# Kernel tuning notes

Measured on AMD Instinct MI355X. Metric: run time of the kernel, lower is better.

## Reference

```python
import jax, jax.numpy as jnp
import numpy as np

IN_DIM, HID, OUT, N_EXTRA, NTASKS, BATCH = 1024, 2048, 10, 3, 10, 4096
LOGSTD_MEAN, LOGSTD_STD = -6.0, 0.1


def setup_inputs() -> dict:
    key = jax.random.key(0)
    ks = jax.random.split(key, 20)
    n = lambda k, s: jax.random.normal(k, s, dtype=jnp.float32)
    return {
        "x": n(ks[0], (BATCH, IN_DIM)),
        # shared layer 0 (in_dim -> hidden)
        "mu_w0": n(ks[1], (HID, IN_DIM)) * (1.0 / np.sqrt(IN_DIM)),
        "ls_w0": LOGSTD_MEAN + LOGSTD_STD * n(ks[2], (HID, IN_DIM)),
        "mu_b0": n(ks[3], (HID,)) * 0.01,
        "ls_b0": LOGSTD_MEAN + LOGSTD_STD * n(ks[4], (HID,)),
        # shared layers 1..3 (hidden -> hidden), stacked
        "mu_w": n(ks[5], (N_EXTRA, HID, HID)) * (1.0 / np.sqrt(HID)),
        "ls_w": LOGSTD_MEAN + LOGSTD_STD * n(ks[6], (N_EXTRA, HID, HID)),
        "mu_b": n(ks[7], (N_EXTRA, HID)) * 0.01,
        "ls_b": LOGSTD_MEAN + LOGSTD_STD * n(ks[8], (N_EXTRA, HID)),
        # per-task heads (hidden -> out), stacked over tasks
        "mu_hw": n(ks[9], (NTASKS, OUT, HID)) * (1.0 / np.sqrt(HID)),
        "ls_hw": LOGSTD_MEAN + LOGSTD_STD * n(ks[10], (NTASKS, OUT, HID)),
        "mu_hb": n(ks[11], (NTASKS, OUT)) * 0.01,
        "ls_hb": LOGSTD_MEAN + LOGSTD_STD * n(ks[12], (NTASKS, OUT)),
        # reparameterization noise (one sample per forward, as in torch module)
        "eps_w0": n(ks[13], (HID, IN_DIM)),
        "eps_b0": n(ks[14], (HID,)),
        "eps_w": n(ks[15], (N_EXTRA, HID, HID)),
        "eps_b": n(ks[16], (N_EXTRA, HID)),
        "eps_hw": n(ks[17], (NTASKS, OUT, HID)),
        "eps_hb": n(ks[18], (NTASKS, OUT)),
        "task": jax.random.randint(ks[19], (BATCH,), 0, NTASKS, dtype=jnp.int64),
    }


def reference(x, mu_w0, ls_w0, mu_b0, ls_b0, mu_w, ls_w, mu_b, ls_b,
              mu_hw, ls_hw, mu_hb, ls_hb,
              eps_w0, eps_b0, eps_w, eps_b, eps_hw, eps_hb, task):
    # BayesianLinear: w = mu + exp(log_sigma) * eps
    w0 = mu_w0 + jnp.exp(ls_w0) * eps_w0          # [HID, IN]
    b0 = mu_b0 + jnp.exp(ls_b0) * eps_b0          # [HID]
    h = jax.nn.relu(x @ w0.T + b0)                # [B, HID]
    for i in range(N_EXTRA):                      # fixed small layer loop
        wi = mu_w[i] + jnp.exp(ls_w[i]) * eps_w[i]
        bi = mu_b[i] + jnp.exp(ls_b[i]) * eps_b[i]
        h = jax.nn.relu(h @ wi.T + bi)
    # multihead: compute every head, zero out non-matching rows (dense masked)
    hw = mu_hw + jnp.exp(ls_hw) * eps_hw          # [T, OUT, HID]
    hb = mu_hb + jnp.exp(ls_hb) * eps_hb          # [T, OUT]
    out_all = jnp.einsum('bh,toh->bto', h, hw) + hb[None]   # [B, T, OUT]
    onehot = (task[:, None] == jnp.arange(NTASKS)[None, :]).astype(h.dtype)
    return jnp.einsum('bto,bt->bo', out_all, onehot)        # [B, OUT]
```

## Files before the change

kernel.cpp:

```cpp
#include <hip/hip_runtime.h>
#include <cstdint>

#define BATCH 4096
#define IN_DIM 1024
#define HID 2048
#define OUT_DIM 10
#define NTASKS 10

typedef __bf16 bf16x8 __attribute__((ext_vector_type(8)));
typedef float f32x4 __attribute__((ext_vector_type(4)));
typedef __attribute__((address_space(3))) uint8_t lds_u8;
typedef const __attribute__((address_space(1))) uint8_t glb_u8;

__device__ __forceinline__ unsigned short f2bf(float f) {
    uint32_t u = __builtin_bit_cast(uint32_t, f);
    u += 0x7fffu + ((u >> 16) & 1u);
    return (unsigned short)(u >> 16);
}

#define C1 1048576u
#define C2 1572864u
#define C3 4718592u
#define C4 4769792u
#define C5 4770304u
#define GLL(src, ldsp) __builtin_amdgcn_global_load_lds((glb_u8*)(src), (lds_u8*)(ldsp), 16, 0, 0)

__global__ __launch_bounds__(256) void bl_stream(
    const float4* __restrict__ x4,
    const float4* __restrict__ m0, const float4* __restrict__ l0, const float4* __restrict__ e0,
    const float4* __restrict__ mw, const float4* __restrict__ lw, const float4* __restrict__ ew,
    const float4* __restrict__ mh, const float4* __restrict__ lh, const float4* __restrict__ eh,
    const float4* __restrict__ mb0, const float4* __restrict__ lb0, const float4* __restrict__ eb0,
    const float4* __restrict__ mb, const float4* __restrict__ lb, const float4* __restrict__ eb,
    const float* __restrict__ mu_hb, const float* __restrict__ ls_hb, const float* __restrict__ eps_hb,
    ushort4* __restrict__ xbf4, ushort4* __restrict__ w0b4, ushort4* __restrict__ wb4,
    float4* __restrict__ hw4, float4* __restrict__ b04, float4* __restrict__ bb4,
    float* __restrict__ hbf)
{
    __shared__ uint8_t sbuf[24576];
    const int tid = threadIdx.x, wv = tid >> 6, ln = tid & 63;

    if (blockIdx.x == 0 && tid < 100)
        hbf[tid] = mu_hb[tid] + __expf(ls_hb[tid]) * eps_hb[tid];

    const int w = blockIdx.x * 4 + wv;
    const int niter = 18 + (w < 832 ? 1 : 0);
    const uint32_t u0 = (uint32_t)(w * 18 + (w < 832 ? w : 832)) * 64u + (uint32_t)ln;
    uint8_t* wl = sbuf + wv * 6144;

    #define SEG_SRC(u, pa, pb, pc)                                               \
        do {                                                                     \
            uint32_t _u = (u);                                                   \
            if (_u < C1)      { pa = x4 + _u; pb = pa; pc = pa; }                \
            else if (_u < C2) { uint32_t v = _u - C1; pa = m0 + v; pb = l0 + v; pc = e0 + v; } \
            else if (_u < C3) { uint32_t v = _u - C2; pa = mw + v; pb = lw + v; pc = ew + v; } \
            else if (_u < C4) { uint32_t v = _u - C3; pa = mh + v; pb = lh + v; pc = eh + v; } \
            else if (_u < C5) { uint32_t v = _u - C4; pa = mb0 + v; pb = lb0 + v; pc = eb0 + v; } \
            else              { uint32_t v = _u - C5; pa = mb + v; pb = lb + v; pc = eb + v; } \
        } while (0)

    {
        const float4 *pa, *pb, *pc;
        SEG_SRC(u0, pa, pb, pc);
        GLL(pa, wl); GLL(pb, wl + 1024); GLL(pc, wl + 2048);
    }

    for (int it = 0; it < niter; ++it) {
        const int cb = it & 1;
        if (it + 1 < niter) {
            const float4 *pa, *pb, *pc;
            SEG_SRC(u0 + (uint32_t)(it + 1) * 64u, pa, pb, pc);
            uint8_t* nb = wl + (cb ^ 1) * 3072;
            GLL(pa, nb); GLL(pb, nb + 1024); GLL(pc, nb + 2048);
            asm volatile("s_waitcnt vmcnt(3)" ::: "memory");
        } else {
            asm volatile("s_waitcnt vmcnt(0)" ::: "memory");
        }
        const uint8_t* rb = wl + cb * 3072;
        const float4 m = *(const float4*)(rb + ln * 16);
        const float4 l = *(const float4*)(rb + 1024 + ln * 16);
        const float4 e = *(const float4*)(rb + 2048 + ln * 16);

        const uint32_t u = u0 + (uint32_t)it * 64u;
        if (u < C1) {
            ushort4 r;
            r.x = f2bf(m.x); r.y = f2bf(m.y); r.z = f2bf(m.z); r.w = f2bf(m.w);
            xbf4[u] = r;
        } else {
            float4 t;
            t.x = m.x + __expf(l.x) * e.x;
            t.y = m.y + __expf(l.y) * e.y;
            t.z = m.z + __expf(l.z) * e.z;
            t.w = m.w + __expf(l.w) * e.w;
            if (u < C3) {
                ushort4 r;
                r.x = f2bf(t.x); r.y = f2bf(t.y); r.z = f2bf(t.z); r.w = f2bf(t.w);
                if (u < C2) w0b4[u - C1] = r; else wb4[u - C2] = r;
            } else {
                if (u < C4) hw4[u - C3] = t;
                else if (u < C5) b04[u - C4] = t;
                else bb4[u - C5] = t;
            }
        }
    }
    #undef SEG_SRC
}

#define BAR()        asm volatile("s_barrier" ::: "memory")
#define WAIT_LGKM0() do { asm volatile("s_waitcnt lgkmcnt(0)" ::: "memory"); __builtin_amdgcn_sched_barrier(0); } while (0)
#define RD_A(m, o)   (*(const bf16x8*)(ldsb + acur + (o) + (m)*2048))
#define RD_B(n, o)   (*(const bf16x8*)(ldsb + bcur + (o) + (n)*2048))
#define MFMA(d, va, vb) d = __builtin_amdgcn_mfma_f32_16x16x32_bf16(va, vb, d, 0, 0, 0)
#define STAGEI(i, kel, sl) \
    __builtin_amdgcn_global_load_lds((glb_u8*)(gsrc[i] + (kel)), \
        (lds_u8*)(ldsb + ldst[i] + (uint32_t)(sl) * smul[i]), 16, 0, 0)

__global__ __launch_bounds__(512, 2) void bl_gemm(
    const unsigned short* __restrict__ A,
    const unsigned short* __restrict__ B,
    const float* __restrict__ bias,
    unsigned short* __restrict__ C,
    int K)
{
    __shared__ unsigned short lds[49152];
    uint8_t* ldsb = (uint8_t*)lds;

    const int tid  = threadIdx.x;
    const int wave = tid >> 6;
    const int lane = tid & 63;
    const int swz = ((blockIdx.x & 7) << 5) | (blockIdx.x >> 3);
    const int bm = swz >> 4;
    const int bn = swz & 15;
    const int wr = wave >> 1;
    const int wc = wave & 1;

    const int lr8 = lane >> 3;
    const int ss  = (lane & 7) ^ lr8;
    const unsigned short* gsrc[6];
    uint32_t ldst[6], smul[6];
    #pragma unroll
    for (int i = 0; i < 6; ++i) {
        const int c = wave * 6 + i;
        if (c < 32) {
            gsrc[i] = A + (size_t)(bm * 256 + c * 8 + lr8) * K + ss * 8;
            ldst[i] = (uint32_t)c * 1024u;
            smul[i] = 32768u;
        } else {
            gsrc[i] = B + (size_t)(bn * 128 + (c - 32) * 8 + lr8) * K + ss * 8;
            ldst[i] = 65536u + (uint32_t)(c - 32) * 1024u;
            smul[i] = 16384u;
        }
    }

    const int rA = wr * 64 + (lane & 15);
    const int rB = wc * 64 + (lane & 15);
    const int ks = lane >> 4;
    const uint32_t aoff0 = (uint32_t)(rA * 128 + ((ks       ^ (rA & 7)) * 16));
    const uint32_t aoff1 = (uint32_t)(rA * 128 + (((4 | ks) ^ (rA & 7)) * 16));
    const uint32_t boff0 = (uint32_t)(rB * 128 + ((ks       ^ (rB & 7)) * 16));
    const uint32_t boff1 = (uint32_t)(rB * 128 + (((4 | ks) ^ (rB & 7)) * 16));

    f32x4 acc[4][4] = {};
    const int NT = K >> 6;

    STAGEI(0, 0, 0); STAGEI(1, 0, 0); STAGEI(2, 0, 0);
    STAGEI(3, 0, 0); STAGEI(4, 0, 0); STAGEI(5, 0, 0);
    __syncthreads();

    for (int t = 0; t < NT; ++t) {
        const int cur = t & 1, nxt = cur ^ 1;
        const uint32_t acur = (uint32_t)cur * 32768u;
        const uint32_t bcur = 65536u + (uint32_t)cur * 16384u;
        const bool pf = (t + 1 < NT);
        const int ktn = (t + 1) << 6;

        bf16x8 a0, a1, a2, a3, b0, b1, b2, b3;

        a0 = RD_A(0, aoff0); a1 = RD_A(1, aoff0);
        b0 = RD_B(0, boff0); b1 = RD_B(1, boff0); b2 = RD_B(2, boff0); b3 = RD_B(3, boff0);
        if (pf) { STAGEI(0, ktn, nxt); STAGEI(1, ktn, nxt); STAGEI(2, ktn, nxt); }
        BAR(); WAIT_LGKM0();
        __builtin_amdgcn_s_setprio(1);
        MFMA(acc[0][0], a0, b0); MFMA(acc[0][1], a0, b1); MFMA(acc[0][2], a0, b2); MFMA(acc[0][3], a0, b3);
        MFMA(acc[1][0], a1, b0); MFMA(acc[1][1], a1, b1); MFMA(acc[1][2], a1, b2); MFMA(acc[1][3], a1, b3);
        __builtin_amdgcn_s_setprio(0);
        BAR();

        a2 = RD_A(2, aoff0); a3 = RD_A(3, aoff0);
        if (pf) { STAGEI(3, ktn, nxt); STAGEI(4, ktn, nxt); STAGEI(5, ktn, nxt); }
        BAR(); WAIT_LGKM0();
        __builtin_amdgcn_s_setprio(1);
        MFMA(acc[2][0], a2, b0); MFMA(acc[2][1], a2, b1); MFMA(acc[2][2], a2, b2); MFMA(acc[2][3], a2, b3);
        MFMA(acc[3][0], a3, b0); MFMA(acc[3][1], a3, b1); MFMA(acc[3][2], a3, b2); MFMA(acc[3][3], a3, b3);
        __builtin_amdgcn_s_setprio(0);
        BAR();

        a0 = RD_A(0, aoff1); a1 = RD_A(1, aoff1);
        b0 = RD_B(0, boff1); b1 = RD_B(1, boff1); b2 = RD_B(2, boff1); b3 = RD_B(3, boff1);
        BAR(); WAIT_LGKM0();
        __builtin_amdgcn_s_setprio(1);
        MFMA(acc[0][0], a0, b0); MFMA(acc[0][1], a0, b1); MFMA(acc[0][2], a0, b2); MFMA(acc[0][3], a0, b3);
        MFMA(acc[1][0], a1, b0); MFMA(acc[1][1], a1, b1); MFMA(acc[1][2], a1, b2); MFMA(acc[1][3], a1, b3);
        __builtin_amdgcn_s_setprio(0);
        BAR();

        a2 = RD_A(2, aoff1); a3 = RD_A(3, aoff1);
        BAR(); WAIT_LGKM0();
        __builtin_amdgcn_s_setprio(1);
        MFMA(acc[2][0], a2, b0); MFMA(acc[2][1], a2, b1); MFMA(acc[2][2], a2, b2); MFMA(acc[2][3], a2, b3);
        MFMA(acc[3][0], a3, b0); MFMA(acc[3][1], a3, b1); MFMA(acc[3][2], a3, b2); MFMA(acc[3][3], a3, b3);
        __builtin_amdgcn_s_setprio(0);
        __syncthreads();
    }

    const int col0 = bn * 128 + wc * 64 + (lane & 15);
    const int row0 = bm * 256 + wr * 64 + ((lane >> 4) << 2);
    #pragma unroll
    for (int n = 0; n < 4; ++n) {
        const int col = col0 + n * 16;
        const float bv = bias[col];
        #pragma unroll
        for (int m = 0; m < 4; ++m) {
            #pragma unroll
            for (int j = 0; j < 4; ++j) {
                float v = acc[m][n][j] + bv;
                v = v > 0.0f ? v : 0.0f;
                C[(size_t)(row0 + m * 16 + j) * HID + col] = f2bf(v);
            }
        }
    }
}

__global__ __launch_bounds__(256) void bl_head(
    const unsigned short* __restrict__ h,
    const float* __restrict__ hw,
    const float* __restrict__ hb,
    const int* __restrict__ task,
    float* __restrict__ out)
{
    const int wave = threadIdx.x >> 6, lane = threadIdx.x & 63;
    const int b = blockIdx.x * 4 + wave;
    const int t = task[b];
    const float* w = hw + (size_t)t * OUT_DIM * HID;
    const unsigned short* hr = h + (size_t)b * HID;

    float acc[OUT_DIM];
    #pragma unroll
    for (int o = 0; o < OUT_DIM; ++o) acc[o] = 0.0f;

    #pragma unroll
    for (int i = 0; i < HID / 512; ++i) {
        const int k0 = (i * 64 + lane) * 8;
        const bf16x8 hv8 = *(const bf16x8*)(hr + k0);
        float hf[8];
        #pragma unroll
        for (int j = 0; j < 8; ++j) hf[j] = (float)hv8[j];
        #pragma unroll
        for (int o = 0; o < OUT_DIM; ++o) {
            const float4 w0 = *(const float4*)(w + (size_t)o * HID + k0);
            const float4 w1 = *(const float4*)(w + (size_t)o * HID + k0 + 4);
            acc[o] += hf[0]*w0.x + hf[1]*w0.y + hf[2]*w0.z + hf[3]*w0.w
                    + hf[4]*w1.x + hf[5]*w1.y + hf[6]*w1.z + hf[7]*w1.w;
        }
    }
    #pragma unroll
    for (int o = 0; o < OUT_DIM; ++o) {
        float v = acc[o];
        #pragma unroll
        for (int s = 32; s > 0; s >>= 1) v += __shfl_down(v, s, 64);
        if (lane == 0) out[(size_t)b * OUT_DIM + o] = v + hb[t * OUT_DIM + o];
    }
}


extern "C" void kernel_launch(void* const* d_in, const int* in_sizes, int n_in,
                              void* d_out, int out_size, void* d_ws, size_t ws_size,
                              hipStream_t stream)
{
    const float* x      = (const float*)d_in[0];
    const float* mu_w0  = (const float*)d_in[1];
    const float* ls_w0  = (const float*)d_in[2];
    const float* mu_b0  = (const float*)d_in[3];
    const float* ls_b0  = (const float*)d_in[4];
    const float* mu_w   = (const float*)d_in[5];
    const float* ls_w   = (const float*)d_in[6];
    const float* mu_b   = (const float*)d_in[7];
    const float* ls_b   = (const float*)d_in[8];
    const float* mu_hw  = (const float*)d_in[9];
    const float* ls_hw  = (const float*)d_in[10];
    const float* mu_hb  = (const float*)d_in[11];
    const float* ls_hb  = (const float*)d_in[12];
    const float* eps_w0 = (const float*)d_in[13];
    const float* eps_b0 = (const float*)d_in[14];
    const float* eps_w  = (const float*)d_in[15];
    const float* eps_b  = (const float*)d_in[16];
    const float* eps_hw = (const float*)d_in[17];
    const float* eps_hb = (const float*)d_in[18];
    const int*   task   = (const int*)d_in[19];

    uint8_t* ws = (uint8_t*)d_ws;
    constexpr size_t HH     = (size_t)HID * HID;
    constexpr size_t X_OFF  = 0;
    constexpr size_t W0_OFF = X_OFF  + (size_t)BATCH * IN_DIM * 2;
    constexpr size_t W_OFF  = W0_OFF + (size_t)HID * IN_DIM * 2;
    constexpr size_t H0_OFF = W_OFF  + 3 * HH * 2;
    constexpr size_t H1_OFF = H0_OFF + (size_t)BATCH * HID * 2;
    constexpr size_t B_OFF  = H1_OFF + (size_t)BATCH * HID * 2;
    constexpr size_t HW_OFF = B_OFF  + (size_t)4 * HID * 4;
    constexpr size_t HB_OFF = HW_OFF + (size_t)NTASKS * OUT_DIM * HID * 4;

    unsigned short* xbf = (unsigned short*)(ws + X_OFF);
    unsigned short* w0b = (unsigned short*)(ws + W0_OFF);
    unsigned short* wb  = (unsigned short*)(ws + W_OFF);
    unsigned short* h0  = (unsigned short*)(ws + H0_OFF);
    unsigned short* h1  = (unsigned short*)(ws + H1_OFF);
    float* ball = (float*)(ws + B_OFF);
    float* hwf  = (float*)(ws + HW_OFF);
    float* hbf  = (float*)(ws + HB_OFF);

    bl_stream<<<1024, 256, 0, stream>>>(
        (const float4*)x,
        (const float4*)mu_w0, (const float4*)ls_w0, (const float4*)eps_w0,
        (const float4*)mu_w,  (const float4*)ls_w,  (const float4*)eps_w,
        (const float4*)mu_hw, (const float4*)ls_hw, (const float4*)eps_hw,
        (const float4*)mu_b0, (const float4*)ls_b0, (const float4*)eps_b0,
        (const float4*)mu_b,  (const float4*)ls_b,  (const float4*)eps_b,
        mu_hb, ls_hb, eps_hb,
        (ushort4*)xbf, (ushort4*)w0b, (ushort4*)wb,
        (float4*)hwf, (float4*)ball, (float4*)(ball + HID), hbf);

    bl_gemm<<<256, 512, 0, stream>>>(xbf, w0b, ball,             h0, IN_DIM);
    bl_gemm<<<256, 512, 0, stream>>>(h0, wb,                     ball + HID,   h1, HID);
    bl_gemm<<<256, 512, 0, stream>>>(h1, wb + HH,                ball + 2*HID, h0, HID);
    bl_gemm<<<256, 512, 0, stream>>>(h0, wb + 2*HH,              ball + 3*HID, h1, HID);

    bl_head<<<BATCH / 4, 256, 0, stream>>>(h1, hwf, hbf, task, (float*)d_out);
}
```

Baseline: 209.0 us.

## Fuse weight reparameterization and x conversion into GEMM operand loading

Drops the separate streaming kernel that materialized bf16 weights and bf16 x in workspace. Each GEMM now reads mu/logsigma/eps fp32 for its B tile straight into registers, computes mu+exp(ls)*eps, packs to bf16 and writes to LDS. The first GEMM likewise converts fp32 x on the fly. This removes a full write and re-read of the sampled weights, but every GEMM block recomputes the weight transform (16 M-blocks each redo it), reads three fp32 streams instead of one bf16 stream, and launch bounds drop to one block per SM.

```diff
diff --git a/kernel.cpp b/kernel.cpp
--- a/kernel.cpp
+++ b/kernel.cpp
@@ -17,93 +17,46 @@
     u += 0x7fffu + ((u >> 16) & 1u);
     return (unsigned short)(u >> 16);
 }
-
-#define C1 1048576u
-#define C2 1572864u
-#define C3 4718592u
-#define C4 4769792u
-#define C5 4770304u
-#define GLL(src, ldsp) __builtin_amdgcn_global_load_lds((glb_u8*)(src), (lds_u8*)(ldsp), 16, 0, 0)
-
-__global__ __launch_bounds__(256) void bl_stream(
-    const float4* __restrict__ x4,
-    const float4* __restrict__ m0, const float4* __restrict__ l0, const float4* __restrict__ e0,
-    const float4* __restrict__ mw, const float4* __restrict__ lw, const float4* __restrict__ ew,
+__device__ __forceinline__ uint32_t pk(float a, float b) {
+    return (uint32_t)f2bf(a) | ((uint32_t)f2bf(b) << 16);
+}
+__device__ __forceinline__ uint4 tf8(float4 ma, float4 mb, float4 la, float4 lb,
+                                     float4 ea, float4 eb) {
+    uint4 r;
+    r.x = pk(ma.x + __expf(la.x) * ea.x, ma.y + __expf(la.y) * ea.y);
+    r.y = pk(ma.z + __expf(la.z) * ea.z, ma.w + __expf(la.w) * ea.w);
+    r.z = pk(mb.x + __expf(lb.x) * eb.x, mb.y + __expf(lb.y) * eb.y);
+    r.w = pk(mb.z + __expf(lb.z) * eb.z, mb.w + __expf(lb.w) * eb.w);
+    return r;
+}
+__device__ __forceinline__ uint4 cv8(float4 a, float4 b) {
+    uint4 r;
+    r.x = pk(a.x, a.y); r.y = pk(a.z, a.w);
+    r.z = pk(b.x, b.y); r.w = pk(b.z, b.w);
+    return r;
+}
+
+__global__ __launch_bounds__(256) void bl_smallx(
     const float4* __restrict__ mh, const float4* __restrict__ lh, const float4* __restrict__ eh,
     const float4* __restrict__ mb0, const float4* __restrict__ lb0, const float4* __restrict__ eb0,
     const float4* __restrict__ mb, const float4* __restrict__ lb, const float4* __restrict__ eb,
     const float* __restrict__ mu_hb, const float* __restrict__ ls_hb, const float* __restrict__ eps_hb,
-    ushort4* __restrict__ xbf4, ushort4* __restrict__ w0b4, ushort4* __restrict__ wb4,
     float4* __restrict__ hw4, float4* __restrict__ b04, float4* __restrict__ bb4,
     float* __restrict__ hbf)
 {
-    __shared__ uint8_t sbuf[24576];
-    const int tid = threadIdx.x, wv = tid >> 6, ln = tid & 63;
-
-    if (blockIdx.x == 0 && tid < 100)
-        hbf[tid] = mu_hb[tid] + __expf(ls_hb[tid]) * eps_hb[tid];
-
-    const int w = blockIdx.x * 4 + wv;
-    const int niter = 18 + (w < 832 ? 1 : 0);
-    const uint32_t u0 = (uint32_t)(w * 18 + (w < 832 ? w : 832)) * 64u + (uint32_t)ln;
-    uint8_t* wl = sbuf + wv * 6144;
-
-    #define SEG_SRC(u, pa, pb, pc)                                               \
-        do {                                                                     \
-            uint32_t _u = (u);                                                   \
-            if (_u < C1)      { pa = x4 + _u; pb = pa; pc = pa; }                \
-            else if (_u < C2) { uint32_t v = _u - C1; pa = m0 + v; pb = l0 + v; pc = e0 + v; } \
-            else if (_u < C3) { uint32_t v = _u - C2; pa = mw + v; pb = lw + v; pc = ew + v; } \
-            else if (_u < C4) { uint32_t v = _u - C3; pa = mh + v; pb = lh + v; pc = eh + v; } \
-            else if (_u < C5) { uint32_t v = _u - C4; pa = mb0 + v; pb = lb0 + v; pc = eb0 + v; } \
-            else              { uint32_t v = _u - C5; pa = mb + v; pb = lb + v; pc = eb + v; } \
-        } while (0)
-
-    {
-        const float4 *pa, *pb, *pc;
-        SEG_SRC(u0, pa, pb, pc);
-        GLL(pa, wl); GLL(pb, wl + 1024); GLL(pc, wl + 2048);
-    }
-
-    for (int it = 0; it < niter; ++it) {
-        const int cb = it & 1;
-        if (it + 1 < niter) {
-            const float4 *pa, *pb, *pc;
-            SEG_SRC(u0 + (uint32_t)(it + 1) * 64u, pa, pb, pc);
-            uint8_t* nb = wl + (cb ^ 1) * 3072;
-            GLL(pa, nb); GLL(pb, nb + 1024); GLL(pc, nb + 2048);
-            asm volatile("s_waitcnt vmcnt(3)" ::: "memory");
-        } else {
-            asm volatile("s_waitcnt vmcnt(0)" ::: "memory");
-        }
-        const uint8_t* rb = wl + cb * 3072;
-        const float4 m = *(const float4*)(rb + ln * 16);
-        const float4 l = *(const float4*)(rb + 1024 + ln * 16);
-        const float4 e = *(const float4*)(rb + 2048 + ln * 16);
-
-        const uint32_t u = u0 + (uint32_t)it * 64u;
-        if (u < C1) {
-            ushort4 r;
-            r.x = f2bf(m.x); r.y = f2bf(m.y); r.z = f2bf(m.z); r.w = f2bf(m.w);
-            xbf4[u] = r;
-        } else {
-            float4 t;
-            t.x = m.x + __expf(l.x) * e.x;
-            t.y = m.y + __expf(l.y) * e.y;
-            t.z = m.z + __expf(l.z) * e.z;
-            t.w = m.w + __expf(l.w) * e.w;
-            if (u < C3) {
-                ushort4 r;
-                r.x = f2bf(t.x); r.y = f2bf(t.y); r.z = f2bf(t.z); r.w = f2bf(t.w);
-                if (u < C2) w0b4[u - C1] = r; else wb4[u - C2] = r;
-            } else {
-                if (u < C4) hw4[u - C3] = t;
-                else if (u < C5) b04[u - C4] = t;
-                else bb4[u - C5] = t;
-            }
-        }
-    }
-    #undef SEG_SRC
+    const uint32_t u = blockIdx.x * 256 + threadIdx.x;
+    if (blockIdx.x == 0 && threadIdx.x < 100)
+        hbf[threadIdx.x] = mu_hb[threadIdx.x] + __expf(ls_hb[threadIdx.x]) * eps_hb[threadIdx.x];
+    float4 m, l, e; float4* dst;
+    if (u < 51200u)      { m = mh[u]; l = lh[u]; e = eh[u]; dst = hw4 + u; }
+    else if (u < 51712u) { const uint32_t v = u - 51200u; m = mb0[v]; l = lb0[v]; e = eb0[v]; dst = b04 + v; }
+    else                 { const uint32_t v = u - 51712u; m = mb[v];  l = lb[v];  e = eb[v];  dst = bb4 + v; }
+    float4 r;
+    r.x = m.x + __expf(l.x) * e.x;
+    r.y = m.y + __expf(l.y) * e.y;
+    r.z = m.z + __expf(l.z) * e.z;
+    r.w = m.w + __expf(l.w) * e.w;
+    *dst = r;
 }
 
 #define BAR()        asm volatile("s_barrier" ::: "memory")
@@ -111,13 +64,20 @@
 #define RD_A(m, o)   (*(const bf16x8*)(ldsb + acur + (o) + (m)*2048))
 #define RD_B(n, o)   (*(const bf16x8*)(ldsb + bcur + (o) + (n)*2048))
 #define MFMA(d, va, vb) d = __builtin_amdgcn_mfma_f32_16x16x32_bf16(va, vb, d, 0, 0, 0)
-#define STAGEI(i, kel, sl) \
-    __builtin_amdgcn_global_load_lds((glb_u8*)(gsrc[i] + (kel)), \
-        (lds_u8*)(ldsb + ldst[i] + (uint32_t)(sl) * smul[i]), 16, 0, 0)
-
-__global__ __launch_bounds__(512, 2) void bl_gemm(
-    const unsigned short* __restrict__ A,
-    const unsigned short* __restrict__ B,
+#define STAGEA(i, kel, sl) \
+    __builtin_amdgcn_global_load_lds((glb_u8*)(gA[i] + (kel)), \
+        (lds_u8*)(ldsb + (uint32_t)(wave * 4 + (i)) * 1024u + (uint32_t)(sl) * 32768u), 16, 0, 0)
+#define LOADB0(k4) do { Bm0a = gBm0[k4]; Bm0b = gBm0[(k4)+1]; Bl0a = gBl0[k4]; \
+    Bl0b = gBl0[(k4)+1]; Be0a = gBe0[k4]; Be0b = gBe0[(k4)+1]; } while (0)
+#define LOADB1(k4) do { Bm1a = gBm1[k4]; Bm1b = gBm1[(k4)+1]; Bl1a = gBl1[k4]; \
+    Bl1b = gBl1[(k4)+1]; Be1a = gBe1[k4]; Be1b = gBe1[(k4)+1]; } while (0)
+#define WRB0(sl) (*(uint4*)(ldsb + bD0 + (uint32_t)(sl) * 16384u) = tf8(Bm0a, Bm0b, Bl0a, Bl0b, Be0a, Be0b))
+#define WRB1(sl) (*(uint4*)(ldsb + bD1 + (uint32_t)(sl) * 16384u) = tf8(Bm1a, Bm1b, Bl1a, Bl1b, Be1a, Be1b))
+
+template <bool AF32>
+__global__ __launch_bounds__(512, 1) void bl_gemm(
+    const void* __restrict__ Ap,
+    const float4* __restrict__ Bm4, const float4* __restrict__ Bl4, const float4* __restrict__ Be4,
     const float* __restrict__ bias,
     unsigned short* __restrict__ C,
     int K)
@@ -133,24 +93,31 @@
     const int bn = swz & 15;
     const int wr = wave >> 1;
     const int wc = wave & 1;
-
     const int lr8 = lane >> 3;
     const int ss  = (lane & 7) ^ lr8;
-    const unsigned short* gsrc[6];
-    uint32_t ldst[6], smul[6];
-    #pragma unroll
-    for (int i = 0; i < 6; ++i) {
-        const int c = wave * 6 + i;
-        if (c < 32) {
-            gsrc[i] = A + (size_t)(bm * 256 + c * 8 + lr8) * K + ss * 8;
-            ldst[i] = (uint32_t)c * 1024u;
-            smul[i] = 32768u;
-        } else {
-            gsrc[i] = B + (size_t)(bn * 128 + (c - 32) * 8 + lr8) * K + ss * 8;
-            ldst[i] = 65536u + (uint32_t)(c - 32) * 1024u;
-            smul[i] = 16384u;
-        }
-    }
+    const int K4  = K >> 2;
+
+    const unsigned short* gA[4];
+    const float4* gAf[4];
+    #pragma unroll
+    for (int i = 0; i < 4; ++i) {
+        const int ca = wave * 4 + i;
+        const int row = bm * 256 + ca * 8 + lr8;
+        if constexpr (AF32) gAf[i] = (const float4*)Ap + (size_t)row * K4 + ss * 2;
+        else                gA[i]  = (const unsigned short*)Ap + (size_t)row * K + ss * 8;
+    }
+    const int cb0 = wave * 2, cb1 = wave * 2 + 1;
+    const int rB0 = bn * 128 + cb0 * 8 + lr8;
+    const int rB1 = bn * 128 + cb1 * 8 + lr8;
+    const float4* gBm0 = Bm4 + (size_t)rB0 * K4 + ss * 2;
+    const float4* gBl0 = Bl4 + (size_t)rB0 * K4 + ss * 2;
+    const float4* gBe0 = Be4 + (size_t)rB0 * K4 + ss * 2;
+    const float4* gBm1 = Bm4 + (size_t)rB1 * K4 + ss * 2;
+    const float4* gBl1 = Bl4 + (size_t)rB1 * K4 + ss * 2;
+    const float4* gBe1 = Be4 + (size_t)rB1 * K4 + ss * 2;
+    const uint32_t bD0 = 65536u + (uint32_t)cb0 * 1024u + (uint32_t)lane * 16u;
+    const uint32_t bD1 = 65536u + (uint32_t)cb1 * 1024u + (uint32_t)lane * 16u;
+    const uint32_t aD  = (uint32_t)(wave * 4) * 1024u + (uint32_t)lane * 16u;
 
     const int rA = wr * 64 + (lane & 15);
     const int rB = wc * 64 + (lane & 15);
@@ -163,8 +130,24 @@
     f32x4 acc[4][4] = {};
     const int NT = K >> 6;
 
-    STAGEI(0, 0, 0); STAGEI(1, 0, 0); STAGEI(2, 0, 0);
-    STAGEI(3, 0, 0); STAGEI(4, 0, 0); STAGEI(5, 0, 0);
+    float4 Bm0a, Bm0b, Bl0a, Bl0b, Be0a, Be0b;
+    float4 Bm1a, Bm1b, Bl1a, Bl1b, Be1a, Be1b;
+    float4 Aa0, Ab0, Aa1, Ab1, Aa2, Ab2, Aa3, Ab3;
+
+    LOADB0(0); LOADB1(0);
+    if constexpr (AF32) {
+        Aa0 = gAf[0][0]; Ab0 = gAf[0][1]; Aa1 = gAf[1][0]; Ab1 = gAf[1][1];
+        Aa2 = gAf[2][0]; Ab2 = gAf[2][1]; Aa3 = gAf[3][0]; Ab3 = gAf[3][1];
+    } else {
+        STAGEA(0, 0, 0); STAGEA(1, 0, 0); STAGEA(2, 0, 0); STAGEA(3, 0, 0);
+    }
+    WRB0(0); WRB1(0);
+    if constexpr (AF32) {
+        *(uint4*)(ldsb + aD)         = cv8(Aa0, Ab0);
+        *(uint4*)(ldsb + aD + 1024u) = cv8(Aa1, Ab1);
+        *(uint4*)(ldsb + aD + 2048u) = cv8(Aa2, Ab2);
+        *(uint4*)(ldsb + aD + 3072u) = cv8(Aa3, Ab3);
+    }
     __syncthreads();
 
     for (int t = 0; t < NT; ++t) {
@@ -172,13 +155,14 @@
         const uint32_t acur = (uint32_t)cur * 32768u;
         const uint32_t bcur = 65536u + (uint32_t)cur * 16384u;
         const bool pf = (t + 1 < NT);
+        const int k4n = (t + 1) * 16;
         const int ktn = (t + 1) << 6;
 
         bf16x8 a0, a1, a2, a3, b0, b1, b2, b3;
 
+        if (pf) { LOADB0(k4n); LOADB1(k4n); }
         a0 = RD_A(0, aoff0); a1 = RD_A(1, aoff0);
         b0 = RD_B(0, boff0); b1 = RD_B(1, boff0); b2 = RD_B(2, boff0); b3 = RD_B(3, boff0);
-        if (pf) { STAGEI(0, ktn, nxt); STAGEI(1, ktn, nxt); STAGEI(2, ktn, nxt); }
         BAR(); WAIT_LGKM0();
         __builtin_amdgcn_s_setprio(1);
         MFMA(acc[0][0], a0, b0); MFMA(acc[0][1], a0, b1); MFMA(acc[0][2], a0, b2); MFMA(acc[0][3], a0, b3);
@@ -186,8 +170,18 @@
         __builtin_amdgcn_s_setprio(0);
         BAR();
 
+        if (pf) {
+            if constexpr (AF32) {
+                Aa0 = gAf[0][k4n]; Ab0 = gAf[0][k4n + 1];
+                Aa1 = gAf[1][k4n]; Ab1 = gAf[1][k4n + 1];
+                Aa2 = gAf[2][k4n]; Ab2 = gAf[2][k4n + 1];
+                Aa3 = gAf[3][k4n]; Ab3 = gAf[3][k4n + 1];
+            } else {
+                STAGEA(0, ktn, nxt); STAGEA(1, ktn, nxt);
+                STAGEA(2, ktn, nxt); STAGEA(3, ktn, nxt);
+            }
+        }
         a2 = RD_A(2, aoff0); a3 = RD_A(3, aoff0);
-        if (pf) { STAGEI(3, ktn, nxt); STAGEI(4, ktn, nxt); STAGEI(5, ktn, nxt); }
         BAR(); WAIT_LGKM0();
         __builtin_amdgcn_s_setprio(1);
         MFMA(acc[2][0], a2, b0); MFMA(acc[2][1], a2, b1); MFMA(acc[2][2], a2, b2); MFMA(acc[2][3], a2, b3);
@@ -202,6 +196,7 @@
         MFMA(acc[0][0], a0, b0); MFMA(acc[0][1], a0, b1); MFMA(acc[0][2], a0, b2); MFMA(acc[0][3], a0, b3);
         MFMA(acc[1][0], a1, b0); MFMA(acc[1][1], a1, b1); MFMA(acc[1][2], a1, b2); MFMA(acc[1][3], a1, b3);
         __builtin_amdgcn_s_setprio(0);
+        if (pf) WRB0(nxt);
         BAR();
 
         a2 = RD_A(2, aoff1); a3 = RD_A(3, aoff1);
@@ -210,6 +205,16 @@
         MFMA(acc[2][0], a2, b0); MFMA(acc[2][1], a2, b1); MFMA(acc[2][2], a2, b2); MFMA(acc[2][3], a2, b3);
         MFMA(acc[3][0], a3, b0); MFMA(acc[3][1], a3, b1); MFMA(acc[3][2], a3, b2); MFMA(acc[3][3], a3, b3);
         __builtin_amdgcn_s_setprio(0);
+        if (pf) {
+            WRB1(nxt);
+            if constexpr (AF32) {
+                const uint32_t ad = aD + (uint32_t)nxt * 32768u;
+                *(uint4*)(ldsb + ad)         = cv8(Aa0, Ab0);
+                *(uint4*)(ldsb + ad + 1024u) = cv8(Aa1, Ab1);
+                *(uint4*)(ldsb + ad + 2048u) = cv8(Aa2, Ab2);
+                *(uint4*)(ldsb + ad + 3072u) = cv8(Aa3, Ab3);
+            }
+        }
         __syncthreads();
     }
 
@@ -299,40 +304,38 @@
     const int*   task   = (const int*)d_in[19];
 
     uint8_t* ws = (uint8_t*)d_ws;
-    constexpr size_t HH     = (size_t)HID * HID;
-    constexpr size_t X_OFF  = 0;
-    constexpr size_t W0_OFF = X_OFF  + (size_t)BATCH * IN_DIM * 2;
-    constexpr size_t W_OFF  = W0_OFF + (size_t)HID * IN_DIM * 2;
-    constexpr size_t H0_OFF = W_OFF  + 3 * HH * 2;
+    constexpr size_t HH4    = (size_t)HID * HID / 4;
+    constexpr size_t H0_OFF = 0;
     constexpr size_t H1_OFF = H0_OFF + (size_t)BATCH * HID * 2;
     constexpr size_t B_OFF  = H1_OFF + (size_t)BATCH * HID * 2;
     constexpr size_t HW_OFF = B_OFF  + (size_t)4 * HID * 4;
     constexpr size_t HB_OFF = HW_OFF + (size_t)NTASKS * OUT_DIM * HID * 4;
 
-    unsigned short* xbf = (unsigned short*)(ws + X_OFF);
-    unsigned short* w0b = (unsigned short*)(ws + W0_OFF);
-    unsigned short* wb  = (unsigned short*)(ws + W_OFF);
     unsigned short* h0  = (unsigned short*)(ws + H0_OFF);
     unsigned short* h1  = (unsigned short*)(ws + H1_OFF);
     float* ball = (float*)(ws + B_OFF);
     float* hwf  = (float*)(ws + HW_OFF);
     float* hbf  = (float*)(ws + HB_OFF);
 
-    bl_stream<<<1024, 256, 0, stream>>>(
-        (const float4*)x,
-        (const float4*)mu_w0, (const float4*)ls_w0, (const float4*)eps_w0,
-        (const float4*)mu_w,  (const float4*)ls_w,  (const float4*)eps_w,
+    bl_smallx<<<208, 256, 0, stream>>>(
         (const float4*)mu_hw, (const float4*)ls_hw, (const float4*)eps_hw,
         (const float4*)mu_b0, (const float4*)ls_b0, (const float4*)eps_b0,
         (const float4*)mu_b,  (const float4*)ls_b,  (const float4*)eps_b,
         mu_hb, ls_hb, eps_hb,
-        (ushort4*)xbf, (ushort4*)w0b, (ushort4*)wb,
         (float4*)hwf, (float4*)ball, (float4*)(ball + HID), hbf);
 
-    bl_gemm<<<256, 512, 0, stream>>>(xbf, w0b, ball,             h0, IN_DIM);
-    bl_gemm<<<256, 512, 0, stream>>>(h0, wb,                     ball + HID,   h1, HID);
-    bl_gemm<<<256, 512, 0, stream>>>(h1, wb + HH,                ball + 2*HID, h0, HID);
-    bl_gemm<<<256, 512, 0, stream>>>(h0, wb + 2*HH,              ball + 3*HID, h1, HID);
+    bl_gemm<true><<<256, 512, 0, stream>>>(
+        x, (const float4*)mu_w0, (const float4*)ls_w0, (const float4*)eps_w0,
+        ball, h0, IN_DIM);
+    bl_gemm<false><<<256, 512, 0, stream>>>(
+        h0, (const float4*)mu_w, (const float4*)ls_w, (const float4*)eps_w,
+        ball + HID, h1, HID);
+    bl_gemm<false><<<256, 512, 0, stream>>>(
+        h1, (const float4*)mu_w + HH4, (const float4*)ls_w + HH4, (const float4*)eps_w + HH4,
+        ball + 2 * HID, h0, HID);
+    bl_gemm<false><<<256, 512, 0, stream>>>(
+        h0, (const float4*)mu_w + 2 * HH4, (const float4*)ls_w + 2 * HH4, (const float4*)eps_w + 2 * HH4,
+        ball + 3 * HID, h1, HID);
 
     bl_head<<<BATCH / 4, 256, 0, stream>>>(h1, hwf, hbf, task, (float*)d_out);
 }
```

Result: slower. 446.8 us (+113.7%).
